# Kernel tuning notes

Measured on AMD Instinct MI355X. Metric: run time of the kernel, lower is better.

Reference implementation:

```python
import jax, jax.numpy as jnp
import numpy as np

H = 8            # num heads
K_ORDER = 3      # polynomial filter order


def setup_inputs() -> dict:
    key = jax.random.key(0)
    ks = jax.random.split(key, 7)
    B, N, D = 4, 2048, 256
    s = 0.05  # weight scale to keep softmax/poly numerically tame
    x = jax.random.normal(ks[0], (B, N, D), jnp.float32)
    Wq = jax.random.normal(ks[1], (D, D), jnp.float32) * s
    Wk = jax.random.normal(ks[2], (D, D), jnp.float32) * s
    Wv = jax.random.normal(ks[3], (D, D), jnp.float32) * s
    Wo = jax.random.normal(ks[4], (D, D), jnp.float32) * s
    coeffs = jax.random.normal(ks[5], (H, K_ORDER + 1), jnp.float32) * 0.5
    z = jnp.zeros((D,), jnp.float32)
    return {"x": x, "Wq": Wq, "bq": z, "Wk": Wk, "bk": z,
            "Wv": Wv, "bv": z, "Wo": Wo, "bo": z, "coeffs": coeffs}


def reference(x, Wq, bq, Wk, bk, Wv, bv, Wo, bo, coeffs):
    B, N, D = x.shape
    hd = D // H

    def split_heads(t):  # [B,N,D] -> [B,H,N,hd]
        return t.reshape(B, N, H, hd).transpose(0, 2, 1, 3)

    q = split_heads(x @ Wq + bq)
    k = split_heads(x @ Wk + bk)
    v = split_heads(x @ Wv + bv)

    # Estimator: learned adjacency via scaled-dot-product softmax, [B,H,N,N]
    scale = jnp.asarray(1.0 / np.sqrt(hd), x.dtype)
    A = jax.nn.softmax(jnp.einsum('bhnd,bhmd->bhnm', q, k) * scale, axis=-1)

    # Filter: X' = sum_{k=0}^{K} c[h,k] * A^k V
    out = coeffs[None, :, 0, None, None] * v
    t = v
    for kk in range(1, K_ORDER + 1):
        t = jnp.einsum('bhnm,bhmd->bhnd', A, t)
        out = out + coeffs[None, :, kk, None, None] * t

    merged = out.transpose(0, 2, 1, 3).reshape(B, N, D)  # concat heads
    return merged @ Wo + bo
```

## Files before the change

kernel.cpp:

```cpp
#include <hip/hip_runtime.h>
#include <hip/hip_bf16.h>

typedef __hip_bfloat16 bf16;
typedef __attribute__((ext_vector_type(8))) short short8;
typedef __attribute__((ext_vector_type(4))) short short4v;
typedef __attribute__((ext_vector_type(4))) float f32x4;

#define BB 4
#define NN 2048
#define DD 256
#define HH 8
#define HD 32
#define BN (BB*NN)
#define ELEMS (BN*DD)

__device__ __attribute__((aligned(256))) unsigned short g_xb [ELEMS];
__device__ __attribute__((aligned(256))) unsigned short g_qb [ELEMS];
__device__ __attribute__((aligned(256))) unsigned short g_kb [ELEMS];
__device__ __attribute__((aligned(256))) unsigned short g_tA [ELEMS];
__device__ __attribute__((aligned(256))) unsigned short g_tB [ELEMS];
__device__ __attribute__((aligned(256))) float          g_acc[ELEMS];
__device__ __attribute__((aligned(256))) unsigned short g_mg [ELEMS];
__device__ __attribute__((aligned(256))) unsigned short g_wt [4*DD*DD];
__device__ __attribute__((aligned(256))) float g_bias[4*DD];
__device__ __attribute__((aligned(256))) float g_cf[HH*4];
__device__ __attribute__((aligned(256))) float g_invl[BB*HH*NN];

__device__ __forceinline__ float b2f(unsigned short u) {
    union { unsigned int i; float f; } c; c.i = ((unsigned int)u) << 16; return c.f;
}
__device__ __forceinline__ unsigned short f2b(float f) {
    bf16 h = __float2bfloat16(f);
    return *reinterpret_cast<unsigned short*>(&h);
}
#if __has_builtin(__builtin_amdgcn_cvt_pk_bf16_f32)
typedef __attribute__((ext_vector_type(2))) __bf16 bf16x2t;
__device__ __forceinline__ unsigned int pk2(float a, float b) {
    union { bf16x2t v; unsigned int u; } c;
    c.v = __builtin_amdgcn_cvt_pk_bf16_f32(a, b);
    return c.u;
}
#else
__device__ __forceinline__ unsigned int pk2(float a, float b) {
    unsigned int ua = __float_as_uint(a), ub = __float_as_uint(b);
    ua = (ua + 0x7FFFu + ((ua >> 16) & 1u)) >> 16;
    ub = (ub + 0x7FFFu + ((ub >> 16) & 1u)) & 0xFFFF0000u;
    return ua | ub;
}
#endif
__device__ __forceinline__ float ldin(const void* p, int i, int f32m) {
    return f32m ? ((const float*)p)[i] : b2f(((const unsigned short*)p)[i]);
}

#if __has_builtin(__builtin_amdgcn_global_load_lds)
#define HAS_GLL 1
typedef const __attribute__((address_space(1))) unsigned int* gas_t;
typedef __attribute__((address_space(3))) unsigned int* las_t;
__device__ __forceinline__ void gll16(const void* gsrc, void* ldst) {
    __builtin_amdgcn_global_load_lds((gas_t)gsrc, (las_t)ldst, 16, 0, 0);
}
#else
#define HAS_GLL 0
#endif

__device__ __forceinline__ int block_probe(const void* x, int tid, int nthr)
{
    __shared__ int cnt;
    if (tid == 0) cnt = 0;
    __syncthreads();
    const unsigned short* u = (const unsigned short*)x;
    int w = 0;
    for (int i = tid; i < 1024; i += nthr) {
        const int e = (u[2 * i] >> 7) & 0xFF;
        if (e < 100 || e > 140) ++w;
    }
    if (w) atomicAdd(&cnt, w);
    __syncthreads();
    return cnt > 300;
}

__global__ __launch_bounds__(256) void prep_kernel(
    const void* __restrict__ x,
    const void* W0, const void* W1, const void* W2, const void* W3,
    const void* bq, const void* bk, const void* bv, const void* bo,
    const void* coeffs)
{
    const int t = threadIdx.x;
    const int f32m = block_probe(x, t, 256);

    if (blockIdx.x < 1024) {
        const size_t i0 = ((size_t)blockIdx.x * 256 + t) * 8;
        if (f32m) {
            const float4 a = *(const float4*)((const float*)x + i0);
            const float4 b = *(const float4*)((const float*)x + i0 + 4);
            union { uint4 v; unsigned int u[4]; } o;
            o.u[0] = pk2(a.x, a.y); o.u[1] = pk2(a.z, a.w);
            o.u[2] = pk2(b.x, b.y); o.u[3] = pk2(b.z, b.w);
            *(uint4*)(g_xb + i0) = o.v;
        } else {
            *(uint4*)(g_xb + i0) = *(const uint4*)((const unsigned short*)x + i0);
        }
        return;
    }

    __shared__ unsigned short tile[64][65];
    const int bi  = blockIdx.x - 1024;
    const int mat = bi >> 4;
    const int bx  = bi & 15;
    const void* W = (mat == 0) ? W0 : (mat == 1) ? W1 : (mat == 2) ? W2 : W3;
    const int k0 = (bx >> 2) * 64;
    const int n0 = (bx & 3) * 64;

    if (bi == 0) {
        g_bias[0 * DD + t] = ldin(bq, t, f32m);
        g_bias[1 * DD + t] = ldin(bk, t, f32m);
        g_bias[2 * DD + t] = ldin(bv, t, f32m);
        g_bias[3 * DD + t] = ldin(bo, t, f32m);
        if (t < 32) g_cf[t] = ldin(coeffs, t, f32m);
    }

    #pragma unroll
    for (int it = 0; it < 16; ++it) {
        const int flat = it * 256 + t;
        const int i = flat >> 6, j = flat & 63;
        tile[j][i] = f2b(ldin(W, (k0 + i) * DD + n0 + j, f32m));
    }
    __syncthreads();
    unsigned short* wt = g_wt + mat * DD * DD;
    #pragma unroll
    for (int it = 0; it < 16; ++it) {
        const int flat = it * 256 + t;
        const int nl = flat >> 6, kl = flat & 63;
        wt[(n0 + nl) * DD + k0 + kl] = tile[nl][kl];
    }
}

__global__ __launch_bounds__(256) void qkv_gemm_kernel()
{
    __shared__ unsigned short xs[128 * 32];
    __shared__ unsigned short wl[64 * 32];
    const int t  = threadIdx.x;
    const int w  = t >> 6, l = t & 63, lg = l >> 4, ln = l & 15;
    const int wm = w >> 1, wn = w & 1;
    const int r0 = blockIdx.x * 128;
    const int n0 = blockIdx.y * 64;
    const int mat = blockIdx.z;
    const unsigned short* wt = g_wt + mat * DD * DD;

    f32x4 acc[4][2];
    #pragma unroll
    for (int m = 0; m < 4; ++m)
        #pragma unroll
        for (int s = 0; s < 2; ++s) acc[m][s] = (f32x4){0,0,0,0};

    for (int kc = 0; kc < DD; kc += 32) {
        __syncthreads();
#if HAS_GLL
        #pragma unroll
        for (int c = 0; c < 2; ++c) {
            const int s = c * 256 + t;
            gll16(g_xb + (size_t)(r0 + (s >> 2)) * DD + kc + (s & 3) * 8,
                  xs + (s >> 2) * 32 + (s & 3) * 8);
        }
        gll16(wt + (size_t)(n0 + (t >> 2)) * DD + kc + (t & 3) * 8,
              wl + (t >> 2) * 32 + (t & 3) * 8);
#else
        #pragma unroll
        for (int c = 0; c < 2; ++c) {
            const int s = c * 256 + t;
            *(uint4*)(xs + (s >> 2) * 32 + (s & 3) * 8) =
                *(const uint4*)(g_xb + (size_t)(r0 + (s >> 2)) * DD + kc + (s & 3) * 8);
        }
        *(uint4*)(wl + (t >> 2) * 32 + (t & 3) * 8) =
            *(const uint4*)(wt + (size_t)(n0 + (t >> 2)) * DD + kc + (t & 3) * 8);
#endif
        __syncthreads();

        short8 af[4];
        #pragma unroll
        for (int m = 0; m < 4; ++m)
            af[m] = *(const short8*)(xs + (wm * 64 + m * 16 + ln) * 32 + lg * 8);
        #pragma unroll
        for (int s = 0; s < 2; ++s) {
            const short8 bfr = *(const short8*)(wl + (wn * 32 + s * 16 + ln) * 32 + lg * 8);
            #pragma unroll
            for (int m = 0; m < 4; ++m)
                acc[m][s] = __builtin_amdgcn_mfma_f32_16x16x32_bf16(af[m], bfr, acc[m][s], 0, 0, 0);
        }
    }

    const float QS = 0.17677669529663687f * 1.4426950408889634f;
    #pragma unroll
    for (int s = 0; s < 2; ++s) {
        const int j = n0 + wn * 32 + s * 16 + ln;
        const float bias = g_bias[mat * DD + j];
        const int h = j >> 5, dd = j & 31;
        #pragma unroll
        for (int m = 0; m < 4; ++m) {
            #pragma unroll
            for (int r = 0; r < 4; ++r) {
                const int rn = r0 + wm * 64 + m * 16 + lg * 4 + r;
                const int b = rn >> 11, n = rn & (NN - 1);
                const int bh = b * HH + h;
                const float val = acc[m][s][r] + bias;
                if (mat == 0) {
                    g_qb[((size_t)bh * NN + n) * HD + dd] = f2b(val * QS);
                } else if (mat == 1) {
                    g_kb[((size_t)bh * NN + n) * HD + dd] = f2b(val);
                } else {
                    g_tA[((size_t)bh * HD + dd) * NN + n] = f2b(val);
                    g_acc[(size_t)rn * DD + j] = g_cf[h * 4] * val;
                }
            }
        }
    }
}

#define KSP 40
#define TSP 136
template<int KIND>
__global__ __launch_bounds__(512, 1) void attn_pass_kernel(const int kidx, const int dir)
{
    __shared__ unsigned short ks[2][128 * KSP];
    __shared__ unsigned short ts[2][32 * TSP];

    const unsigned short* __restrict__ tin  = dir ? g_tB : g_tA;
    unsigned short*       __restrict__ tout = dir ? g_tA : g_tB;

    const int tid = threadIdx.x;
    const int w   = tid >> 6;
    const int l   = tid & 63;
    const int lg  = l >> 4;
    const int ln  = l & 15;

    const int bi = blockIdx.x;
    const int bh = (bi & 7) * 4 + ((bi >> 3) & 3);
    const int qt = bi >> 5;
    const int h  = bh & (HH - 1);
    const int b  = bh >> 3;
    const int q0 = qt * 128;
    const int qw = q0 + w * 16;

    const short8 qf = *(const short8*)(g_qb +
        ((size_t)bh * NN + qw + ln) * HD + lg * 8);

    const unsigned short* kb = g_kb + (size_t)bh * NN * HD;
    const unsigned short* tb = tin  + (size_t)bh * HD * NN;

    const f32x4 zero = {0.f, 0.f, 0.f, 0.f};
    f32x4 o0e = zero, o0o = zero, o1e = zero, o1o = zero;
    float lsum = 0.f;

    const int krow = tid >> 2, kcol = (tid & 3) * 8;
    const int trow = tid >> 4, tcol = (tid & 15) * 8;

    uint4 krg = *(const uint4*)(kb + tid * 8);
    uint4 trg = *(const uint4*)(tb + (size_t)trow * NN + tcol);
    *(uint4*)(ks[0] + krow * KSP + kcol) = krg;
    *(uint4*)(ts[0] + trow * TSP + tcol) = trg;
    __syncthreads();

    int cur = 0;
    for (int it = 0; it < 16; ++it) {
        if (it < 15) {
            const int k1 = (it + 1) * 128;
            krg = *(const uint4*)(kb + (size_t)k1 * HD + tid * 8);
            trg = *(const uint4*)(tb + (size_t)trow * NN + k1 + tcol);
        }
        const unsigned short* ksc = ks[cur];
        const unsigned short* tsc = ts[cur];

        #pragma unroll
        for (int half = 0; half < 2; ++half) {
            short8 kf[4];
            #pragma unroll
            for (int c = 0; c < 4; ++c)
                kf[c] = *(const short8*)(ksc + ((half * 4 + c) * 16 + ln) * KSP + lg * 8);
            __builtin_amdgcn_s_setprio(1);
            f32x4 s[4];
            #pragma unroll
            for (int c = 0; c < 4; ++c)
                s[c] = __builtin_amdgcn_mfma_f32_16x16x32_bf16(kf[c], qf, zero, 0, 0, 0);
            float p[16];
            #pragma unroll
            for (int c = 0; c < 4; ++c)
                #pragma unroll
                for (int r = 0; r < 4; ++r)
                    p[c * 4 + r] = __builtin_amdgcn_exp2f(s[c][r]);
            if (KIND == 0) {
                #pragma unroll
                for (int e = 0; e < 16; ++e) lsum += p[e];
            }
            #pragma unroll
            for (int c = 0; c < 4; ++c) {
                const int cc = half * 4 + c;
                union { unsigned int u[2]; short4v s4; } pb;
                pb.u[0] = pk2(p[c * 4 + 0], p[c * 4 + 1]);
                pb.u[1] = pk2(p[c * 4 + 2], p[c * 4 + 3]);
                const short4v tf0 = *(const short4v*)(tsc + ln * TSP + cc * 16 + lg * 4);
                const short4v tf1 = *(const short4v*)(tsc + (16 + ln) * TSP + cc * 16 + lg * 4);
                if (cc & 1) {
                    o0o = __builtin_amdgcn_mfma_f32_16x16x16bf16_1k(tf0, pb.s4, o0o, 0, 0, 0);
                    o1o = __builtin_amdgcn_mfma_f32_16x16x16bf16_1k(tf1, pb.s4, o1o, 0, 0, 0);
                } else {
                    o0e = __builtin_amdgcn_mfma_f32_16x16x16bf16_1k(tf0, pb.s4, o0e, 0, 0, 0);
                    o1e = __builtin_amdgcn_mfma_f32_16x16x16bf16_1k(tf1, pb.s4, o1e, 0, 0, 0);
                }
            }
            __builtin_amdgcn_s_setprio(0);
        }

        if (it < 15) {
            *(uint4*)(ks[cur ^ 1] + krow * KSP + kcol) = krg;
            *(uint4*)(ts[cur ^ 1] + trow * TSP + tcol) = trg;
        }
        __syncthreads();
        cur ^= 1;
    }

    const f32x4 oacc0 = o0e + o0o;
    const f32x4 oacc1 = o1e + o1o;

    float invl;
    if (KIND == 0) {
        lsum += __shfl_xor(lsum, 16, 64);
        lsum += __shfl_xor(lsum, 32, 64);
        invl = 1.0f / lsum;
        if (lg == 0) g_invl[(size_t)bh * NN + qw + ln] = invl;
    } else {
        invl = g_invl[(size_t)bh * NN + qw + ln];
    }

    const float ck = g_cf[h * 4 + kidx];
    #pragma unroll
    for (int hf = 0; hf < 2; ++hf) {
        const f32x4& oa = hf ? oacc1 : oacc0;
        #pragma unroll
        for (int r = 0; r < 4; ++r) {
            const int d = hf * 16 + lg * 4 + r;
            const float val = oa[r] * invl;
            const size_t gi = ((size_t)(b * NN + qw + ln)) * DD + h * HD + d;
            if (KIND != 2) {
                tout[((size_t)bh * HD + d) * NN + qw + ln] = f2b(val);
                g_acc[gi] += ck * val;
            } else {
                g_mg[gi] = f2b(g_acc[gi] + ck * val);
            }
        }
    }
}

__global__ __launch_bounds__(256) void out_gemm_kernel(void* __restrict__ out,
                                                       const void* __restrict__ x)
{
    const int t  = threadIdx.x;
    const int f32m = block_probe(x, t, 256);
    __shared__ unsigned short xs[64 * 32];
    __shared__ unsigned short wl[64 * 32];
    const int w  = t >> 6, l = t & 63, lg = l >> 4, ln = l & 15;
    const int r0 = blockIdx.x * 64;
    const int n0 = blockIdx.y * 64;
    const unsigned short* wt = g_wt + 3 * DD * DD;
    const int sr = t >> 2, sc = (t & 3) * 8;

    f32x4 acc[4] = {{0,0,0,0},{0,0,0,0},{0,0,0,0},{0,0,0,0}};

    for (int kc = 0; kc < DD; kc += 32) {
        __syncthreads();
#if HAS_GLL
        gll16(g_mg + (size_t)(r0 + sr) * DD + kc + sc, xs + sr * 32 + sc);
        gll16(wt   + (size_t)(n0 + sr) * DD + kc + sc, wl + sr * 32 + sc);
#else
        *(uint4*)(xs + sr * 32 + sc) =
            *(const uint4*)(g_mg + (size_t)(r0 + sr) * DD + kc + sc);
        *(uint4*)(wl + sr * 32 + sc) =
            *(const uint4*)(wt + (size_t)(n0 + sr) * DD + kc + sc);
#endif
        __syncthreads();
        const short8 af = *(const short8*)(xs + (w * 16 + ln) * 32 + lg * 8);
        #pragma unroll
        for (int s = 0; s < 4; ++s) {
            const short8 bfr = *(const short8*)(wl + (s * 16 + ln) * 32 + lg * 8);
            acc[s] = __builtin_amdgcn_mfma_f32_16x16x32_bf16(af, bfr, acc[s], 0, 0, 0);
        }
    }

    #pragma unroll
    for (int s = 0; s < 4; ++s) {
        const int j = n0 + s * 16 + ln;
        const float bias = g_bias[3 * DD + j];
        #pragma unroll
        for (int r = 0; r < 4; ++r) {
            const int rn = r0 + w * 16 + lg * 4 + r;
            const float val = acc[s][r] + bias;
            if (f32m) ((float*)out)[(size_t)rn * DD + j] = val;
            else      ((bf16*)out)[(size_t)rn * DD + j] = __float2bfloat16(val);
        }
    }
}

extern "C" void kernel_launch(void* const* d_in, const int* in_sizes, int n_in,
                              void* d_out, int out_size, void* d_ws, size_t ws_size,
                              hipStream_t stream)
{
    const void* x      = d_in[0];
    const void* Wq     = d_in[1];
    const void* bq     = d_in[2];
    const void* Wk     = d_in[3];
    const void* bk     = d_in[4];
    const void* Wv     = d_in[5];
    const void* bv     = d_in[6];
    const void* Wo     = d_in[7];
    const void* bo     = d_in[8];
    const void* coeffs = d_in[9];
    (void)d_ws; (void)ws_size; (void)in_sizes; (void)n_in; (void)out_size;

    prep_kernel<<<1088, 256, 0, stream>>>(x, Wq, Wk, Wv, Wo,
                                          bq, bk, bv, bo, coeffs);

    qkv_gemm_kernel<<<dim3(64, 4, 3), 256, 0, stream>>>();

    const int agrid = (BB * HH) * (NN / 128);
    attn_pass_kernel<0><<<agrid, 512, 0, stream>>>(1, 0);
    attn_pass_kernel<1><<<agrid, 512, 0, stream>>>(2, 1);
    attn_pass_kernel<2><<<agrid, 512, 0, stream>>>(3, 0);

    out_gemm_kernel<<<dim3(128, 4), 256, 0, stream>>>(d_out, x);
}
```

Before: 209.4 us.

## Fuse three attention passes into one cooperative kernel with grid sync

Replaces the three separate attention-pass launches with a single cooperative kernel that loops over the three polynomial powers and separates them with grid-wide barriers. Softmax normalizer, Q fragment and the coefficient accumulator stay in registers across passes instead of being reloaded from global memory. Falls back to the three-kernel path if the cooperative launch fails. This removes two kernel-launch gaps and some global traffic, but adds grid.sync overhead and requires all 512 blocks to be co-resident.

```diff
diff --git a/kernel.cpp b/kernel.cpp
--- a/kernel.cpp
+++ b/kernel.cpp
@@ -1,5 +1,8 @@
 #include <hip/hip_runtime.h>
 #include <hip/hip_bf16.h>
+#include <hip/hip_cooperative_groups.h>
+
+namespace cg = cooperative_groups;
 
 typedef __hip_bfloat16 bf16;
 typedef __attribute__((ext_vector_type(8))) short short8;
@@ -218,14 +221,13 @@
 
 #define KSP 40
 #define TSP 136
-template<int KIND>
-__global__ __launch_bounds__(512, 1) void attn_pass_kernel(const int kidx, const int dir)
+
+__global__ __launch_bounds__(512, 1) void attn_fused_kernel(int )
 {
     __shared__ unsigned short ks[2][128 * KSP];
     __shared__ unsigned short ts[2][32 * TSP];
 
-    const unsigned short* __restrict__ tin  = dir ? g_tB : g_tA;
-    unsigned short*       __restrict__ tout = dir ? g_tA : g_tB;
+    cg::grid_group grid = cg::this_grid();
 
     const int tid = threadIdx.x;
     const int w   = tid >> 6;
@@ -243,6 +245,150 @@
 
     const short8 qf = *(const short8*)(g_qb +
         ((size_t)bh * NN + qw + ln) * HD + lg * 8);
+    const unsigned short* kb = g_kb + (size_t)bh * NN * HD;
+
+    const int krow = tid >> 2, kcol = (tid & 3) * 8;
+    const int trow = tid >> 4, tcol = (tid & 15) * 8;
+
+    const f32x4 zero = {0.f, 0.f, 0.f, 0.f};
+    float invl = 0.f;
+    f32x4 aloc0 = zero, aloc1 = zero;
+    const size_t rowi = (size_t)(b * NN + qw + ln) * DD + h * HD;
+
+    for (int p = 0; p < 3; ++p) {
+        const unsigned short* tb = ((p == 1) ? g_tB : g_tA) + (size_t)bh * HD * NN;
+        unsigned short* tout = (p == 1) ? g_tA : g_tB;
+
+        f32x4 o0e = zero, o0o = zero, o1e = zero, o1o = zero;
+        float lsum = 0.f;
+
+        uint4 krg = *(const uint4*)(kb + tid * 8);
+        uint4 trg = *(const uint4*)(tb + (size_t)trow * NN + tcol);
+        *(uint4*)(ks[0] + krow * KSP + kcol) = krg;
+        *(uint4*)(ts[0] + trow * TSP + tcol) = trg;
+        __syncthreads();
+
+        int cur = 0;
+        for (int it = 0; it < 16; ++it) {
+            if (it < 15) {
+                const int k1 = (it + 1) * 128;
+                krg = *(const uint4*)(kb + (size_t)k1 * HD + tid * 8);
+                trg = *(const uint4*)(tb + (size_t)trow * NN + k1 + tcol);
+            }
+            const unsigned short* ksc = ks[cur];
+            const unsigned short* tsc = ts[cur];
+
+            #pragma unroll
+            for (int half = 0; half < 2; ++half) {
+                short8 kf[4];
+                #pragma unroll
+                for (int c = 0; c < 4; ++c)
+                    kf[c] = *(const short8*)(ksc + ((half * 4 + c) * 16 + ln) * KSP + lg * 8);
+                __builtin_amdgcn_s_setprio(1);
+                f32x4 s[4];
+                #pragma unroll
+                for (int c = 0; c < 4; ++c)
+                    s[c] = __builtin_amdgcn_mfma_f32_16x16x32_bf16(kf[c], qf, zero, 0, 0, 0);
+                float pp[16];
+                #pragma unroll
+                for (int c = 0; c < 4; ++c)
+                    #pragma unroll
+                    for (int r = 0; r < 4; ++r)
+                        pp[c * 4 + r] = __builtin_amdgcn_exp2f(s[c][r]);
+                if (p == 0) {
+                    #pragma unroll
+                    for (int e = 0; e < 16; ++e) lsum += pp[e];
+                }
+                #pragma unroll
+                for (int c = 0; c < 4; ++c) {
+                    const int cc = half * 4 + c;
+                    union { unsigned int u[2]; short4v s4; } pb;
+                    pb.u[0] = pk2(pp[c * 4 + 0], pp[c * 4 + 1]);
+                    pb.u[1] = pk2(pp[c * 4 + 2], pp[c * 4 + 3]);
+                    const short4v tf0 = *(const short4v*)(tsc + ln * TSP + cc * 16 + lg * 4);
+                    const short4v tf1 = *(const short4v*)(tsc + (16 + ln) * TSP + cc * 16 + lg * 4);
+                    if (cc & 1) {
+                        o0o = __builtin_amdgcn_mfma_f32_16x16x16bf16_1k(tf0, pb.s4, o0o, 0, 0, 0);
+                        o1o = __builtin_amdgcn_mfma_f32_16x16x16bf16_1k(tf1, pb.s4, o1o, 0, 0, 0);
+                    } else {
+                        o0e = __builtin_amdgcn_mfma_f32_16x16x16bf16_1k(tf0, pb.s4, o0e, 0, 0, 0);
+                        o1e = __builtin_amdgcn_mfma_f32_16x16x16bf16_1k(tf1, pb.s4, o1e, 0, 0, 0);
+                    }
+                }
+                __builtin_amdgcn_s_setprio(0);
+            }
+
+            if (it < 15) {
+                *(uint4*)(ks[cur ^ 1] + krow * KSP + kcol) = krg;
+                *(uint4*)(ts[cur ^ 1] + trow * TSP + tcol) = trg;
+            }
+            __syncthreads();
+            cur ^= 1;
+        }
+
+        if (p == 0) {
+            lsum += __shfl_xor(lsum, 16, 64);
+            lsum += __shfl_xor(lsum, 32, 64);
+            invl = 1.0f / lsum;
+        }
+
+        const f32x4 oacc0 = o0e + o0o;
+        const f32x4 oacc1 = o1e + o1o;
+        const float ck = g_cf[h * 4 + p + 1];
+
+        if (p == 0) {
+            aloc0 = *(const f32x4*)(g_acc + rowi + lg * 4);
+            aloc1 = *(const f32x4*)(g_acc + rowi + 16 + lg * 4);
+        }
+        #pragma unroll
+        for (int hf = 0; hf < 2; ++hf) {
+            const f32x4& oa = hf ? oacc1 : oacc0;
+            f32x4&       al = hf ? aloc1 : aloc0;
+            #pragma unroll
+            for (int r = 0; r < 4; ++r) {
+                const int d = hf * 16 + lg * 4 + r;
+                const float val = oa[r] * invl;
+                if (p < 2) {
+                    tout[((size_t)bh * HD + d) * NN + qw + ln] = f2b(val);
+                    al[r] += ck * val;
+                } else {
+                    g_mg[rowi + d] = f2b(al[r] + ck * val);
+                }
+            }
+        }
+
+        if (p < 2) {
+            __threadfence();
+            grid.sync();
+        }
+    }
+}
+
+template<int KIND>
+__global__ __launch_bounds__(512, 1) void attn_pass_kernel(const int kidx, const int dir)
+{
+    __shared__ unsigned short ks[2][128 * KSP];
+    __shared__ unsigned short ts[2][32 * TSP];
+
+    const unsigned short* __restrict__ tin  = dir ? g_tB : g_tA;
+    unsigned short*       __restrict__ tout = dir ? g_tA : g_tB;
+
+    const int tid = threadIdx.x;
+    const int w   = tid >> 6;
+    const int l   = tid & 63;
+    const int lg  = l >> 4;
+    const int ln  = l & 15;
+
+    const int bi = blockIdx.x;
+    const int bh = (bi & 7) * 4 + ((bi >> 3) & 3);
+    const int qt = bi >> 5;
+    const int h  = bh & (HH - 1);
+    const int b  = bh >> 3;
+    const int q0 = qt * 128;
+    const int qw = q0 + w * 16;
+
+    const short8 qf = *(const short8*)(g_qb +
+        ((size_t)bh * NN + qw + ln) * HD + lg * 8);
 
     const unsigned short* kb = g_kb + (size_t)bh * NN * HD;
     const unsigned short* tb = tin  + (size_t)bh * HD * NN;
@@ -281,22 +427,22 @@
             #pragma unroll
             for (int c = 0; c < 4; ++c)
                 s[c] = __builtin_amdgcn_mfma_f32_16x16x32_bf16(kf[c], qf, zero, 0, 0, 0);
-            float p[16];
+            float pp[16];
             #pragma unroll
             for (int c = 0; c < 4; ++c)
                 #pragma unroll
                 for (int r = 0; r < 4; ++r)
-                    p[c * 4 + r] = __builtin_amdgcn_exp2f(s[c][r]);
+                    pp[c * 4 + r] = __builtin_amdgcn_exp2f(s[c][r]);
             if (KIND == 0) {
                 #pragma unroll
-                for (int e = 0; e < 16; ++e) lsum += p[e];
+                for (int e = 0; e < 16; ++e) lsum += pp[e];
             }
             #pragma unroll
             for (int c = 0; c < 4; ++c) {
                 const int cc = half * 4 + c;
                 union { unsigned int u[2]; short4v s4; } pb;
-                pb.u[0] = pk2(p[c * 4 + 0], p[c * 4 + 1]);
-                pb.u[1] = pk2(p[c * 4 + 2], p[c * 4 + 3]);
+                pb.u[0] = pk2(pp[c * 4 + 0], pp[c * 4 + 1]);
+                pb.u[1] = pk2(pp[c * 4 + 2], pp[c * 4 + 3]);
                 const short4v tf0 = *(const short4v*)(tsc + ln * TSP + cc * 16 + lg * 4);
                 const short4v tf1 = *(const short4v*)(tsc + (16 + ln) * TSP + cc * 16 + lg * 4);
                 if (cc & 1) {
@@ -420,10 +566,16 @@
 
     qkv_gemm_kernel<<<dim3(64, 4, 3), 256, 0, stream>>>();
 
-    const int agrid = (BB * HH) * (NN / 128);
-    attn_pass_kernel<0><<<agrid, 512, 0, stream>>>(1, 0);
-    attn_pass_kernel<1><<<agrid, 512, 0, stream>>>(2, 1);
-    attn_pass_kernel<2><<<agrid, 512, 0, stream>>>(3, 0);
+    static int s_dummy = 0;
+    void* kargs[] = { (void*)&s_dummy };
+    hipError_t ce = hipLaunchCooperativeKernel(
+        (const void*)attn_fused_kernel, dim3(512), dim3(512), kargs, 0, stream);
+    if (ce != hipSuccess) {
+        const int agrid = (BB * HH) * (NN / 128);
+        attn_pass_kernel<0><<<agrid, 512, 0, stream>>>(1, 0);
+        attn_pass_kernel<1><<<agrid, 512, 0, stream>>>(2, 1);
+        attn_pass_kernel<2><<<agrid, 512, 0, stream>>>(3, 0);
+    }
 
     out_gemm_kernel<<<dim3(128, 4), 256, 0, stream>>>(d_out, x);
 }
```

New measurement: 551.0 us. 2.63x slower.

## Double-buffer activation tiles and preload full weight slab in projection GEMMs

Applied to the files above, without the earlier changes.

The QKV and output projection GEMMs now load the block's whole 64x256 weight slice into padded shared memory once, instead of reloading a 64x32 chunk every k-step. Activation tiles are double-buffered so the next chunk is fetched while MFMAs run on the current one, leaving one barrier per iteration instead of two. This adds shared memory per block (about 33KB for weights), which may lower occupancy. The row padding is meant to avoid LDS bank conflicts.

```diff
diff --git a/kernel.cpp b/kernel.cpp
--- a/kernel.cpp
+++ b/kernel.cpp
@@ -135,10 +135,11 @@
     }
 }
 
+#define WLP 264
 __global__ __launch_bounds__(256) void qkv_gemm_kernel()
 {
-    __shared__ unsigned short xs[128 * 32];
-    __shared__ unsigned short wl[64 * 32];
+    __shared__ unsigned short xs[2][128 * 32];
+    __shared__ unsigned short wl[64 * WLP];
     const int t  = threadIdx.x;
     const int w  = t >> 6, l = t & 63, lg = l >> 4, ln = l & 15;
     const int wm = w >> 1, wn = w & 1;
@@ -153,40 +154,66 @@
         #pragma unroll
         for (int s = 0; s < 2; ++s) acc[m][s] = (f32x4){0,0,0,0};
 
-    for (int kc = 0; kc < DD; kc += 32) {
-        __syncthreads();
+    #pragma unroll
+    for (int c = 0; c < 8; ++c) {
+        const int s = c * 256 + t;
+        const int row = s >> 5, col = (s & 31) * 8;
+        *(uint4*)(wl + row * WLP + col) =
+            *(const uint4*)(wt + (size_t)(n0 + row) * DD + col);
+    }
 #if HAS_GLL
-        #pragma unroll
-        for (int c = 0; c < 2; ++c) {
-            const int s = c * 256 + t;
-            gll16(g_xb + (size_t)(r0 + (s >> 2)) * DD + kc + (s & 3) * 8,
-                  xs + (s >> 2) * 32 + (s & 3) * 8);
-        }
-        gll16(wt + (size_t)(n0 + (t >> 2)) * DD + kc + (t & 3) * 8,
-              wl + (t >> 2) * 32 + (t & 3) * 8);
-#else
-        #pragma unroll
-        for (int c = 0; c < 2; ++c) {
-            const int s = c * 256 + t;
-            *(uint4*)(xs + (s >> 2) * 32 + (s & 3) * 8) =
-                *(const uint4*)(g_xb + (size_t)(r0 + (s >> 2)) * DD + kc + (s & 3) * 8);
-        }
-        *(uint4*)(wl + (t >> 2) * 32 + (t & 3) * 8) =
-            *(const uint4*)(wt + (size_t)(n0 + (t >> 2)) * DD + kc + (t & 3) * 8);
-#endif
-        __syncthreads();
-
+    #pragma unroll
+    for (int c = 0; c < 2; ++c) {
+        const int s = c * 256 + t;
+        gll16(g_xb + (size_t)(r0 + (s >> 2)) * DD + (s & 3) * 8,
+              xs[0] + s * 8);
+    }
+#else
+    #pragma unroll
+    for (int c = 0; c < 2; ++c) {
+        const int s = c * 256 + t;
+        *(uint4*)(xs[0] + s * 8) =
+            *(const uint4*)(g_xb + (size_t)(r0 + (s >> 2)) * DD + (s & 3) * 8);
+    }
+#endif
+    __syncthreads();
+
+    int cur = 0;
+    for (int it = 0; it < 8; ++it) {
+        const int kc = it * 32;
+        if (it < 7) {
+            const int kn = kc + 32;
+#if HAS_GLL
+            #pragma unroll
+            for (int c = 0; c < 2; ++c) {
+                const int s = c * 256 + t;
+                gll16(g_xb + (size_t)(r0 + (s >> 2)) * DD + kn + (s & 3) * 8,
+                      xs[cur ^ 1] + s * 8);
+            }
+#else
+            #pragma unroll
+            for (int c = 0; c < 2; ++c) {
+                const int s = c * 256 + t;
+                *(uint4*)(xs[cur ^ 1] + s * 8) =
+                    *(const uint4*)(g_xb + (size_t)(r0 + (s >> 2)) * DD + kn + (s & 3) * 8);
+            }
+#endif
+        }
+
+        const unsigned short* xc = xs[cur];
         short8 af[4];
         #pragma unroll
         for (int m = 0; m < 4; ++m)
-            af[m] = *(const short8*)(xs + (wm * 64 + m * 16 + ln) * 32 + lg * 8);
+            af[m] = *(const short8*)(xc + (wm * 64 + m * 16 + ln) * 32 + lg * 8);
         #pragma unroll
         for (int s = 0; s < 2; ++s) {
-            const short8 bfr = *(const short8*)(wl + (wn * 32 + s * 16 + ln) * 32 + lg * 8);
+            const short8 bfr = *(const short8*)(wl + (wn * 32 + s * 16 + ln) * WLP + kc + lg * 8);
             #pragma unroll
             for (int m = 0; m < 4; ++m)
                 acc[m][s] = __builtin_amdgcn_mfma_f32_16x16x32_bf16(af[m], bfr, acc[m][s], 0, 0, 0);
         }
+        __syncthreads();
+        cur ^= 1;
     }
 
     const float QS = 0.17677669529663687f * 1.4426950408889634f;
@@ -355,34 +382,53 @@
 {
     const int t  = threadIdx.x;
     const int f32m = block_probe(x, t, 256);
-    __shared__ unsigned short xs[64 * 32];
-    __shared__ unsigned short wl[64 * 32];
+    __shared__ unsigned short xs[2][64 * 32];
+    __shared__ unsigned short wl[64 * WLP];
     const int w  = t >> 6, l = t & 63, lg = l >> 4, ln = l & 15;
     const int r0 = blockIdx.x * 64;
     const int n0 = blockIdx.y * 64;
     const unsigned short* wt = g_wt + 3 * DD * DD;
-    const int sr = t >> 2, sc = (t & 3) * 8;
 
     f32x4 acc[4] = {{0,0,0,0},{0,0,0,0},{0,0,0,0},{0,0,0,0}};
 
-    for (int kc = 0; kc < DD; kc += 32) {
+    #pragma unroll
+    for (int c = 0; c < 8; ++c) {
+        const int s = c * 256 + t;
+        const int row = s >> 5, col = (s & 31) * 8;
+        *(uint4*)(wl + row * WLP + col) =
+            *(const uint4*)(wt + (size_t)(n0 + row) * DD + col);
+    }
+#if HAS_GLL
+    gll16(g_mg + (size_t)(r0 + (t >> 2)) * DD + (t & 3) * 8, xs[0] + t * 8);
+#else
+    *(uint4*)(xs[0] + t * 8) =
+        *(const uint4*)(g_mg + (size_t)(r0 + (t >> 2)) * DD + (t & 3) * 8);
+#endif
+    __syncthreads();
+
+    int cur = 0;
+    for (int it = 0; it < 8; ++it) {
+        const int kc = it * 32;
+        if (it < 7) {
+            const int kn = kc + 32;
+#if HAS_GLL
+            gll16(g_mg + (size_t)(r0 + (t >> 2)) * DD + kn + (t & 3) * 8,
+                  xs[cur ^ 1] + t * 8);
+#else
+            *(uint4*)(xs[cur ^ 1] + t * 8) =
+                *(const uint4*)(g_mg + (size_t)(r0 + (t >> 2)) * DD + kn + (t & 3) * 8);
+#endif
+        }
+
+        const unsigned short* xc = xs[cur];
+        const short8 af = *(const short8*)(xc + (w * 16 + ln) * 32 + lg * 8);
+        #pragma unroll
+        for (int s = 0; s < 4; ++s) {
+            const short8 bfr = *(const short8*)(wl + (s * 16 + ln) * WLP + kc + lg * 8);
+            acc[s] = __builtin_amdgcn_mfma_f32_16x16x32_bf16(af, bfr, acc[s], 0, 0, 0);
+        }
         __syncthreads();
-#if HAS_GLL
-        gll16(g_mg + (size_t)(r0 + sr) * DD + kc + sc, xs + sr * 32 + sc);
-        gll16(wt   + (size_t)(n0 + sr) * DD + kc + sc, wl + sr * 32 + sc);
-#else
-        *(uint4*)(xs + sr * 32 + sc) =
-            *(const uint4*)(g_mg + (size_t)(r0 + sr) * DD + kc + sc);
-        *(uint4*)(wl + sr * 32 + sc) =
-            *(const uint4*)(wt + (size_t)(n0 + sr) * DD + kc + sc);
-#endif
-        __syncthreads();
-        const short8 af = *(const short8*)(xs + (w * 16 + ln) * 32 + lg * 8);
-        #pragma unroll
-        for (int s = 0; s < 4; ++s) {
-            const short8 bfr = *(const short8*)(wl + (s * 16 + ln) * 32 + lg * 8);
-            acc[s] = __builtin_amdgcn_mfma_f32_16x16x32_bf16(af, bfr, acc[s], 0, 0, 0);
-        }
+        cur ^= 1;
     }
 
     #pragma unroll
```

Measured after the change: 210.6 us. About the same (+0.6%).
